# Performance work log

Measured on AMD Instinct MI355X. Metric: run time of the kernel, lower is better.

The kernel has to match this reference:

```python
import jax, jax.numpy as jnp
import numpy as np

B, S, H = 16, 4096, 1024

def setup_inputs() -> dict:
    key = jax.random.key(0)
    k1, k2, k3 = jax.random.split(key, 3)
    lstm_output = jax.random.normal(k1, (B, S, H), dtype=jnp.float32)
    # nn.Linear(H, H): weight [H, H] (out, in), bias [H]
    W = jax.random.normal(k2, (H, H), dtype=jnp.float32) * (1.0 / np.sqrt(H))
    b = jax.random.normal(k3, (H,), dtype=jnp.float32) * 0.01
    return {"lstm_output": lstm_output, "W": W, "b": b}

def reference(lstm_output, W, b):
    # energy = tanh(x @ W^T + b)  [B, S, H]
    energy = jnp.tanh(jnp.einsum('bsh,oh->bso', lstm_output, W) + b)
    # softmax over the sequence dim (dim=1), per hidden channel
    scores = jax.nn.softmax(energy, axis=1)
    # weighted-sum pooling over sequence -> [B, H]
    context = jnp.sum(scores * lstm_output, axis=1)
    return context
```

## Files before the change

### kernel.cpp

```cpp
#include <hip/hip_runtime.h>
#include <hip/hip_bf16.h>

#define Bsz  16
#define Sdim 4096
#define Hdim 1024
#define Mtot (Bsz * Sdim)
#define Kdim Hdim
#define Ndim Hdim

#define BM2 256
#define BN2 256
#define MT2 (Mtot / BM2)
#define NT2 (Ndim / BN2)
#define NKT32 (Kdim / 32)

typedef short s16x8 __attribute__((ext_vector_type(8)));
typedef float f32x4 __attribute__((ext_vector_type(4)));

__device__ __forceinline__ unsigned short f2bf(float f) {
  __hip_bfloat16 h = __float2bfloat16(f);
  unsigned short u;
  __builtin_memcpy(&u, &h, 2);
  return u;
}
__device__ __forceinline__ s16x8 cvt8(float4 u, float4 v) {
  s16x8 r;
  r[0] = (short)f2bf(u.x); r[1] = (short)f2bf(u.y);
  r[2] = (short)f2bf(u.z); r[3] = (short)f2bf(u.w);
  r[4] = (short)f2bf(v.x); r[5] = (short)f2bf(v.y);
  r[6] = (short)f2bf(v.z); r[7] = (short)f2bf(v.w);
  return r;
}

__device__ __forceinline__ void gload_lds16(const unsigned short* g, unsigned short* l) {
  __builtin_amdgcn_global_load_lds(
      (const __attribute__((address_space(1))) unsigned int*)g,
      (__attribute__((address_space(3))) unsigned int*)l,
      16, 0, 0);
}

__global__ __launch_bounds__(256) void wconv_kernel(const float* __restrict__ W,
                                                    unsigned short* __restrict__ Wb) {
  int i = blockIdx.x * 256 + threadIdx.x;
  float4 v = reinterpret_cast<const float4*>(W)[i];
  ushort4 o;
  o.x = f2bf(v.x); o.y = f2bf(v.y); o.z = f2bf(v.z); o.w = f2bf(v.w);
  reinterpret_cast<ushort4*>(Wb)[i] = o;
}

__global__ __launch_bounds__(512, 2) void attn_main(
    const float* __restrict__ X,
    const unsigned short* __restrict__ Wb,
    const float* __restrict__ bias,
    float* __restrict__ lpart,
    float* __restrict__ cpart) {
  __shared__ unsigned short Abf[2][BM2 * 32];
  __shared__ unsigned short Bbf[2][BN2 * 32];
  __shared__ float red[2][2][BN2];

  int bid = blockIdx.x;
  int swz = (bid & 7) * (MT2 * NT2 / 8) + (bid >> 3);
  const int mt = swz >> 2;
  const int nt = swz & 3;
  const int m0 = mt * BM2;
  const int n0 = nt * BN2;

  const int tid = threadIdx.x;
  const int l   = tid & 63;
  const int w   = tid >> 6;
  const int wm  = w >> 2;
  const int wn  = w & 3;
  const int lr  = l & 15;
  const int lk  = l >> 4;

  f32x4 acc[8][4];
#pragma unroll
  for (int i = 0; i < 8; i++)
#pragma unroll
    for (int j = 0; j < 4; j++) acc[i][j] = (f32x4){0.f, 0.f, 0.f, 0.f};

  const int ra = tid >> 1;
  const int ch = tid & 1;
  const float* gaP = X + (size_t)(m0 + ra) * Kdim + ch * 16;
  const int xa = (ra >> 1) & 3;
  const int swA0 = ra * 32 + (((ch * 2 + 0) ^ xa) << 3);
  const int swA1 = ra * 32 + (((ch * 2 + 1) ^ xa) << 3);

  const int srow = w * 16 + (l >> 2);
  const int scol = (((l & 3) ^ ((l >> 3) & 3)) << 3);
  const unsigned short* srcB0 = Wb + (size_t)(n0 + srow) * Kdim + scol;

  int offA[2][4], offB[4];
#pragma unroll
  for (int mh = 0; mh < 2; mh++)
#pragma unroll
    for (int j = 0; j < 4; j++) {
      const int r = wm * 128 + mh * 64 + j * 16 + lr;
      offA[mh][j] = r * 32 + ((lk ^ ((r >> 1) & 3)) << 3);
    }
#pragma unroll
  for (int n = 0; n < 4; n++) {
    const int rn = wn * 64 + n * 16 + lr;
    offB[n] = rn * 32 + ((lk ^ ((rn >> 1) & 3)) << 3);
  }

#define STAGE_B(slot, tp) do {                                          \
    unsigned short* d = &Bbf[slot][w * 512];                            \
    const unsigned short* g = srcB0 + (size_t)(tp) * 32;                \
    gload_lds16(g, d);                                                  \
    gload_lds16(g + (size_t)128 * Kdim, d + 4096);                      \
  } while (0)

#define MID_BARRIER() do {                                   \
    asm volatile("" ::: "memory");                           \
    __builtin_amdgcn_s_barrier();                            \
    asm volatile("s_waitcnt lgkmcnt(0)" ::: "memory");       \
    __builtin_amdgcn_sched_barrier(0);                       \
  } while (0)
#define END_BARRIER() do {                                   \
    asm volatile("" ::: "memory");                           \
    __builtin_amdgcn_s_barrier();                            \
  } while (0)

  {
    float4 g0 = *(const float4*)(gaP + 0);
    float4 g1 = *(const float4*)(gaP + 4);
    float4 g2 = *(const float4*)(gaP + 8);
    float4 g3 = *(const float4*)(gaP + 12);
    STAGE_B(0, 0);
    *(s16x8*)&Abf[0][swA0] = cvt8(g0, g1);
    *(s16x8*)&Abf[0][swA1] = cvt8(g2, g3);
  }
  __syncthreads();

  s16x8 bf[4];

  for (int t = 0; t < NKT32; ++t) {
    const int cur = t & 1, nxt = cur ^ 1;
    const unsigned short* As = Abf[cur];
    const unsigned short* Bs = Bbf[cur];
    const bool more = (t + 1 < NKT32);
    s16x8 af[4];
    float4 g0, g1, g2, g3;

#pragma unroll
    for (int j = 0; j < 4; ++j) af[j] = *(const s16x8*)&As[offA[0][j]];
#pragma unroll
    for (int n = 0; n < 4; ++n) bf[n] = *(const s16x8*)&Bs[offB[n]];
    if (more) {
      const float* ap = gaP + (t + 1) * 32;
      g0 = *(const float4*)(ap + 0);
      g1 = *(const float4*)(ap + 4);
      g2 = *(const float4*)(ap + 8);
      g3 = *(const float4*)(ap + 12);
      STAGE_B(nxt, t + 1);
    }
    MID_BARRIER();
    __builtin_amdgcn_s_setprio(1);
#pragma unroll
    for (int j = 0; j < 4; ++j)
#pragma unroll
      for (int n = 0; n < 4; ++n)
        acc[j][n] = __builtin_amdgcn_mfma_f32_16x16x32_bf16(af[j], bf[n], acc[j][n], 0, 0, 0);
    __builtin_amdgcn_s_setprio(0);
    END_BARRIER();

#pragma unroll
    for (int j = 0; j < 4; ++j) af[j] = *(const s16x8*)&As[offA[1][j]];
    if (more) {
      *(s16x8*)&Abf[nxt][swA0] = cvt8(g0, g1);
      *(s16x8*)&Abf[nxt][swA1] = cvt8(g2, g3);
    }
    MID_BARRIER();
    __builtin_amdgcn_s_setprio(1);
#pragma unroll
    for (int j = 0; j < 4; ++j)
#pragma unroll
      for (int n = 0; n < 4; ++n)
        acc[4 + j][n] = __builtin_amdgcn_mfma_f32_16x16x32_bf16(af[j], bf[n], acc[4 + j][n], 0, 0, 0);
    __builtin_amdgcn_s_setprio(0);
    if (more) asm volatile("s_waitcnt vmcnt(0)" ::: "memory");
    END_BARRIER();
  }

  float lsum[4], csum[4];
#pragma unroll
  for (int nr = 0; nr < 4; nr++) {
    const int o = n0 + wn * 64 + nr * 16 + lr;
    const float bv = bias[o];
    float lacc = 0.f, cacc = 0.f;
#pragma unroll
    for (int m8 = 0; m8 < 8; m8++) {
      const int sr = m0 + wm * 128 + (m8 >> 2) * 64 + (m8 & 3) * 16 + lk * 4;
#pragma unroll
      for (int r = 0; r < 4; r++) {
        float e  = acc[m8][nr][r] + bv;
        float t  = __expf(2.f * e);
        float th = 1.f - __fdividef(2.f, t + 1.f);
        float sc = __expf(th);
        float xv = X[(size_t)(sr + r) * Kdim + o];
        lacc += sc;
        cacc += sc * xv;
      }
    }
    lacc += __shfl_xor(lacc, 16); lacc += __shfl_xor(lacc, 32);
    cacc += __shfl_xor(cacc, 16); cacc += __shfl_xor(cacc, 32);
    lsum[nr] = lacc; csum[nr] = cacc;
  }

  if (lk == 0) {
#pragma unroll
    for (int nr = 0; nr < 4; nr++) {
      red[wm][0][wn * 64 + nr * 16 + lr] = lsum[nr];
      red[wm][1][wn * 64 + nr * 16 + lr] = csum[nr];
    }
  }
  __syncthreads();
  if (tid < BN2) {
    float L = red[0][0][tid] + red[1][0][tid];
    float C = red[0][1][tid] + red[1][1][tid];
    lpart[(size_t)mt * Ndim + n0 + tid] = L;
    cpart[(size_t)mt * Ndim + n0 + tid] = C;
  }
}

__global__ __launch_bounds__(256) void finalize_kernel(const float* __restrict__ lpart,
                                                       const float* __restrict__ cpart,
                                                       float* __restrict__ out, int chunks) {
  int i = blockIdx.x * 256 + threadIdx.x;
  int b = i >> 10, o = i & 1023;
  float L = 0.f, C = 0.f;
  for (int sc = 0; sc < chunks; ++sc) {
    size_t idx = (size_t)(b * chunks + sc) * Ndim + o;
    L += lpart[idx];
    C += cpart[idx];
  }
  out[i] = C / L;
}

extern "C" void kernel_launch(void* const* d_in, const int* in_sizes, int n_in,
                              void* d_out, int out_size, void* d_ws, size_t ws_size,
                              hipStream_t stream) {
  const float* X    = (const float*)d_in[0];
  const float* W    = (const float*)d_in[1];
  const float* bias = (const float*)d_in[2];
  float* out = (float*)d_out;

  unsigned short* Wb = (unsigned short*)d_ws;
  float* lpart = (float*)((char*)d_ws + (size_t)Ndim * Kdim * 2);
  float* cpart = lpart + (size_t)MT2 * Ndim;

  wconv_kernel<<<dim3(Ndim * Kdim / 1024), dim3(256), 0, stream>>>(W, Wb);
  attn_main<<<dim3(MT2 * NT2), dim3(512), 0, stream>>>(X, Wb, bias, lpart, cpart);
  finalize_kernel<<<dim3(Bsz * Hdim / 256), dim3(256), 0, stream>>>(lpart, cpart, out,
                                                                    Sdim / BM2);
}
```

Measured before the change: 269.1 us.

## Prefetch X two k-tiles ahead with unrolled even/odd register buffers

Unrolls the K loop by two and keeps two sets of float4 prefetch registers (even/odd), so global loads of X are issued two k-steps ahead instead of one. Partial vmcnt waits (vmcnt(4)) replace full drains, letting the next tile's loads stay in flight across barriers. This hides global memory latency for the fp32 A operand, at the cost of extra VGPRs (16 more floats), which may pressure occupancy at 512 threads × 2 blocks.

Measured after the change: 276.1 us. 1.03x slower.

```diff
diff --git a/kernel.cpp b/kernel.cpp
--- a/kernel.cpp
+++ b/kernel.cpp
@@ -121,65 +121,95 @@
     asm volatile("" ::: "memory");                           \
     __builtin_amdgcn_s_barrier();                            \
   } while (0)
+#define VM4() asm volatile("s_waitcnt vmcnt(4)" ::: "memory")
+#define VM0() asm volatile("s_waitcnt vmcnt(0)" ::: "memory")
+
+#define RD_A(SLOT, MH) do {                                              \
+    _Pragma("unroll")                                                    \
+    for (int j = 0; j < 4; ++j) af[j] = *(const s16x8*)&Abf[SLOT][offA[MH][j]]; \
+  } while (0)
+#define RD_Bf(SLOT) do {                                                 \
+    _Pragma("unroll")                                                    \
+    for (int n = 0; n < 4; ++n) bf[n] = *(const s16x8*)&Bbf[SLOT][offB[n]]; \
+  } while (0)
+#define MFMA16(BASE) do {                                                \
+    __builtin_amdgcn_s_setprio(1);                                       \
+    _Pragma("unroll")                                                    \
+    for (int j = 0; j < 4; ++j)                                          \
+      _Pragma("unroll")                                                  \
+      for (int n = 0; n < 4; ++n)                                        \
+        acc[(BASE) + j][n] = __builtin_amdgcn_mfma_f32_16x16x32_bf16(    \
+            af[j], bf[n], acc[(BASE) + j][n], 0, 0, 0);                  \
+    __builtin_amdgcn_s_setprio(0);                                       \
+  } while (0)
+
+  float4 gEv0, gEv1, gEv2, gEv3;
+  float4 gOd0, gOd1, gOd2, gOd3;
 
   {
-    float4 g0 = *(const float4*)(gaP + 0);
-    float4 g1 = *(const float4*)(gaP + 4);
-    float4 g2 = *(const float4*)(gaP + 8);
-    float4 g3 = *(const float4*)(gaP + 12);
+    float4 a0 = *(const float4*)(gaP + 0);
+    float4 a1 = *(const float4*)(gaP + 4);
+    float4 a2 = *(const float4*)(gaP + 8);
+    float4 a3 = *(const float4*)(gaP + 12);
     STAGE_B(0, 0);
-    *(s16x8*)&Abf[0][swA0] = cvt8(g0, g1);
-    *(s16x8*)&Abf[0][swA1] = cvt8(g2, g3);
-  }
-  __syncthreads();
+    gOd0 = *(const float4*)(gaP + 32);
+    gOd1 = *(const float4*)(gaP + 36);
+    gOd2 = *(const float4*)(gaP + 40);
+    gOd3 = *(const float4*)(gaP + 44);
+    *(s16x8*)&Abf[0][swA0] = cvt8(a0, a1);
+    *(s16x8*)&Abf[0][swA1] = cvt8(a2, a3);
+    VM4();
+    asm volatile("s_waitcnt lgkmcnt(0)" ::: "memory");
+    END_BARRIER();
+  }
 
   s16x8 bf[4];
 
-  for (int t = 0; t < NKT32; ++t) {
-    const int cur = t & 1, nxt = cur ^ 1;
-    const unsigned short* As = Abf[cur];
-    const unsigned short* Bs = Bbf[cur];
-    const bool more = (t + 1 < NKT32);
+  for (int u = 0; u < 16; ++u) {
+    const int t0 = 2 * u;
+    const bool more = (u < 15);
     s16x8 af[4];
-    float4 g0, g1, g2, g3;
-
-#pragma unroll
-    for (int j = 0; j < 4; ++j) af[j] = *(const s16x8*)&As[offA[0][j]];
-#pragma unroll
-    for (int n = 0; n < 4; ++n) bf[n] = *(const s16x8*)&Bs[offB[n]];
+
+    RD_A(0, 0); RD_Bf(0);
+    STAGE_B(1, t0 + 1);
     if (more) {
-      const float* ap = gaP + (t + 1) * 32;
-      g0 = *(const float4*)(ap + 0);
-      g1 = *(const float4*)(ap + 4);
-      g2 = *(const float4*)(ap + 8);
-      g3 = *(const float4*)(ap + 12);
-      STAGE_B(nxt, t + 1);
-    }
-    MID_BARRIER();
-    __builtin_amdgcn_s_setprio(1);
-#pragma unroll
-    for (int j = 0; j < 4; ++j)
-#pragma unroll
-      for (int n = 0; n < 4; ++n)
-        acc[j][n] = __builtin_amdgcn_mfma_f32_16x16x32_bf16(af[j], bf[n], acc[j][n], 0, 0, 0);
-    __builtin_amdgcn_s_setprio(0);
-    END_BARRIER();
-
-#pragma unroll
-    for (int j = 0; j < 4; ++j) af[j] = *(const s16x8*)&As[offA[1][j]];
+      const float* ap = gaP + (t0 + 2) * 32;
+      gEv0 = *(const float4*)(ap + 0);
+      gEv1 = *(const float4*)(ap + 4);
+      gEv2 = *(const float4*)(ap + 8);
+      gEv3 = *(const float4*)(ap + 12);
+    }
+    MID_BARRIER();
+    MFMA16(0);
+    END_BARRIER();
+    RD_A(0, 1);
+    *(s16x8*)&Abf[1][swA0] = cvt8(gOd0, gOd1);
+    *(s16x8*)&Abf[1][swA1] = cvt8(gOd2, gOd3);
+    MID_BARRIER();
+    MFMA16(4);
+    if (more) VM4(); else VM0();
+    END_BARRIER();
+
+    RD_A(1, 0); RD_Bf(1);
     if (more) {
-      *(s16x8*)&Abf[nxt][swA0] = cvt8(g0, g1);
-      *(s16x8*)&Abf[nxt][swA1] = cvt8(g2, g3);
-    }
-    MID_BARRIER();
-    __builtin_amdgcn_s_setprio(1);
-#pragma unroll
-    for (int j = 0; j < 4; ++j)
-#pragma unroll
-      for (int n = 0; n < 4; ++n)
-        acc[4 + j][n] = __builtin_amdgcn_mfma_f32_16x16x32_bf16(af[j], bf[n], acc[4 + j][n], 0, 0, 0);
-    __builtin_amdgcn_s_setprio(0);
-    if (more) asm volatile("s_waitcnt vmcnt(0)" ::: "memory");
+      STAGE_B(0, t0 + 2);
+      const float* ap = gaP + (t0 + 3) * 32;
+      gOd0 = *(const float4*)(ap + 0);
+      gOd1 = *(const float4*)(ap + 4);
+      gOd2 = *(const float4*)(ap + 8);
+      gOd3 = *(const float4*)(ap + 12);
+    }
+    MID_BARRIER();
+    MFMA16(0);
+    END_BARRIER();
+    RD_A(1, 1);
+    if (more) {
+      *(s16x8*)&Abf[0][swA0] = cvt8(gEv0, gEv1);
+      *(s16x8*)&Abf[0][swA1] = cvt8(gEv2, gEv3);
+    }
+    MID_BARRIER();
+    MFMA16(4);
+    if (more) VM4();
     END_BARRIER();
   }
 
```
